# Kernel optimization log

Hardware: AMD Instinct MI355X
Metric: run time of the kernel (lower is better)

## Reference

```python
import jax, jax.numpy as jnp
import numpy as np

K = 3  # kernel_size; stride=1, dilation=1, SAME padding (pad=1 each side)


def _aggregation(input_, weight):
    # input_: [n, H, W, c_x] NHWC; weight: [n, c_w, k^2, L] with L = H*W (= c_w here)
    n, H, W, c_x = input_.shape
    c_w = weight.shape[3]  # faithful to tf.shape(weight)[3] in the source
    L = H * W
    # tf.image.extract_patches(..., 'SAME') with k=3, s=1, d=1 -> pad 1 on each spatial side,
    # depth ordered as (ki, kj, channel) flattened, channel fastest.
    xp = jnp.pad(input_, ((0, 0), (1, 1), (1, 1), (0, 0)))
    patches = jnp.stack(
        [xp[:, i:i + H, j:j + W, :] for i in range(K) for j in range(K)],
        axis=3,
    )  # [n, H, W, k^2, c_x]
    unfold = patches.reshape(n, H, W, K * K * c_x)  # == tf.image.extract_patches output
    # Faithful raw reshape (reinterpretation of the flat buffer, as in the TF code)
    out = unfold.reshape(n, c_x // c_w, c_w, K * K, L)
    # broadcast multiply by per-pixel weights and reduce over the k^2 axis
    had = jnp.sum(weight[:, None] * out, axis=-2)  # [n, c_x//c_w, c_w, L]
    return had.reshape(n, c_x, H, W)


def setup_inputs() -> dict:
    key = jax.random.key(0)
    k1, k2 = jax.random.split(key)
    input_ = jax.random.normal(k1, (32, 16, 16, 1024), dtype=jnp.float32)
    weight = jax.random.normal(k2, (32, 256, 9, 256), dtype=jnp.float32)
    return {"input_": input_, "weight": weight}


def reference(input_, weight):
    return _aggregation(input_, weight)
```

## Files before the change

### kernel.cpp

```cpp
#include <hip/hip_runtime.h>


__global__ __launch_bounds__(256)
void Aggregation_33320356282418_kernel(const float* __restrict__ input,
                                       const float* __restrict__ weight,
                                       float* __restrict__ out) {
    const int l   = threadIdx.x;
    const int blk = blockIdx.x;
    const int cw  = blk & 255;
    const int n   = blk >> 8;

    const float* wp = weight + ((size_t)(n * 256 + cw) * 9) * 256 + l;
    float wgt[9];
#pragma unroll
    for (int q = 0; q < 9; ++q) wgt[q] = wp[q * 256];

    const int hbase = cw >> 6;
    const int w0    = (cw >> 2) & 15;
    const int t2b   = (cw & 3) * 2304;

    int  cq[9], diq[9], colq[9];
    bool wvalid[9];
#pragma unroll
    for (int q = 0; q < 9; ++q) {
        const int t2 = t2b + q * 256 + l;
        const int p  = t2 >> 10;
        cq[q]  = t2 & 1023;
        const int di = p / 3;
        const int dj = p - di * 3;
        diq[q] = di;
        const int wj = w0 + dj - 1;
        colq[q]   = wj;
        wvalid[q] = (wj >= 0) && (wj < 16);
    }

    const float* inb  = input + (size_t)n * (16 * 16 * 1024);
    float*       outb = out   + ((size_t)(n * 1024) + cw) * 256 + l;

#pragma unroll
    for (int g = 0; g < 4; ++g) {
        float acc = 0.f;
#pragma unroll
        for (int q = 0; q < 9; ++q) {
            const int hi = 4 * g + hbase + diq[q] - 1;
            float v = 0.f;
            if (wvalid[q] && (unsigned)hi < 16u) {
                v = inb[(hi * 16 + colq[q]) * 1024 + cq[q]];
            }
            acc += wgt[q] * v;
        }
        outb[(size_t)g * (256 * 256)] = acc;
    }
}

extern "C" void kernel_launch(void* const* d_in, const int* in_sizes, int n_in,
                              void* d_out, int out_size, void* d_ws, size_t ws_size,
                              hipStream_t stream) {
    const float* input  = (const float*)d_in[0];
    const float* weight = (const float*)d_in[1];
    float* out = (float*)d_out;

    dim3 grid(32 * 256);
    dim3 block(256);
    hipLaunchKernelGGL(Aggregation_33320356282418_kernel, grid, block, 0, stream,
                       input, weight, out);
}
```

Baseline: 150.5 us.

## Vectorize to float4 per thread, pack four cw per block, remap block order

```diff
diff --git a/kernel.cpp b/kernel.cpp
--- a/kernel.cpp
+++ b/kernel.cpp
@@ -5,51 +5,60 @@
 void Aggregation_33320356282418_kernel(const float* __restrict__ input,
                                        const float* __restrict__ weight,
                                        float* __restrict__ out) {
-    const int l   = threadIdx.x;
-    const int blk = blockIdx.x;
-    const int cw  = blk & 255;
-    const int n   = blk >> 8;
+    const int b   = blockIdx.x;
+    const int blk = (b & 7) * 256 + (b >> 3);
 
-    const float* wp = weight + ((size_t)(n * 256 + cw) * 9) * 256 + l;
-    float wgt[9];
-#pragma unroll
-    for (int q = 0; q < 9; ++q) wgt[q] = wp[q * 256];
+    const int cb  = blk & 63;
+    const int n   = blk >> 6;
+    const int tid = threadIdx.x;
+    const int cwi = tid >> 6;
+    const int t   = tid & 63;
+    const int cw  = cb * 4 + cwi;
 
     const int hbase = cw >> 6;
     const int w0    = (cw >> 2) & 15;
-    const int t2b   = (cw & 3) * 2304;
+    const int mb    = 9 * (cw & 3);
 
-    int  cq[9], diq[9], colq[9];
-    bool wvalid[9];
+    const float4* __restrict__ inp4 =
+        (const float4*)(input + (size_t)n * (16 * 16 * 1024));
+    const float4* __restrict__ w4 =
+        (const float4*)(weight + ((size_t)(n * 256 + cw) * 9) * 256);
+    float4* __restrict__ o4 =
+        (float4*)(out + ((size_t)n * 1024 + cw) * 256);
+
+    float4 acc[4];
+#pragma unroll
+    for (int g = 0; g < 4; ++g) acc[g] = make_float4(0.f, 0.f, 0.f, 0.f);
+
 #pragma unroll
     for (int q = 0; q < 9; ++q) {
-        const int t2 = t2b + q * 256 + l;
-        const int p  = t2 >> 10;
-        cq[q]  = t2 & 1023;
+        const int m  = mb + q;
+        const int p  = m >> 2;
         const int di = p / 3;
-        const int dj = p - di * 3;
-        diq[q] = di;
+        const int dj = p - 3 * di;
         const int wj = w0 + dj - 1;
-        colq[q]   = wj;
-        wvalid[q] = (wj >= 0) && (wj < 16);
+        const bool wok = (unsigned)wj < 16u;
+        const int cu = (m & 3) * 64;
+
+        const float4 wq = w4[q * 64 + t];
+
+#pragma unroll
+        for (int g = 0; g < 4; ++g) {
+            const int hi = 4 * g + hbase + di - 1;
+            float4 v = make_float4(0.f, 0.f, 0.f, 0.f);
+            if (wok && (unsigned)hi < 16u) {
+                v = inp4[(hi * 16 + wj) * 256 + cu + t];
+            }
+            acc[g].x = fmaf(wq.x, v.x, acc[g].x);
+            acc[g].y = fmaf(wq.y, v.y, acc[g].y);
+            acc[g].z = fmaf(wq.z, v.z, acc[g].z);
+            acc[g].w = fmaf(wq.w, v.w, acc[g].w);
+        }
     }
-
-    const float* inb  = input + (size_t)n * (16 * 16 * 1024);
-    float*       outb = out   + ((size_t)(n * 1024) + cw) * 256 + l;
 
 #pragma unroll
     for (int g = 0; g < 4; ++g) {
-        float acc = 0.f;
-#pragma unroll
-        for (int q = 0; q < 9; ++q) {
-            const int hi = 4 * g + hbase + diq[q] - 1;
-            float v = 0.f;
-            if (wvalid[q] && (unsigned)hi < 16u) {
-                v = inb[(hi * 16 + colq[q]) * 1024 + cq[q]];
-            }
-            acc += wgt[q] * v;
-        }
-        outb[(size_t)g * (256 * 256)] = acc;
+        o4[g * (256 * 256 / 4) + t] = acc[g];
     }
 }
 
@@ -60,7 +69,7 @@
     const float* weight = (const float*)d_in[1];
     float* out = (float*)d_out;
 
-    dim3 grid(32 * 256);
+    dim3 grid(32 * 64);
     dim3 block(256);
     hipLaunchKernelGGL(Aggregation_33320356282418_kernel, grid, block, 0, stream,
                        input, weight, out);
```

Result: no change. 151.6 us (+0.8%).
